# Kernel optimization log

Measured on AMD Instinct MI355X. Metric: run time of the kernel, lower is better.

## Reference

```python
import jax, jax.numpy as jnp
import numpy as np

D_MODEL = 1024
N_HEADS = 16
D_HEAD = 64
TOTAL = N_HEADS * D_HEAD


def setup_inputs() -> dict:
    key = jax.random.key(0)
    k1, k2, k3 = jax.random.split(key, 3)
    x = jax.random.normal(k1, (2, 2048, D_MODEL), dtype=jnp.float32)
    W_qkv = jax.random.normal(k2, (3 * TOTAL, D_MODEL), dtype=jnp.float32) * 0.02
    W_out = jax.random.normal(k3, (D_MODEL, TOTAL), dtype=jnp.float32) * 0.02
    return {"x": x, "W_qkv": W_qkv, "W_out": W_out}


def reference(x, W_qkv, W_out):
    B, T, D = x.shape
    scale = D_HEAD ** -0.5
    qkv = jnp.einsum('btd,ed->bte', x, W_qkv)  # [B,T,3*TOTAL]
    q, k, v = jnp.split(qkv, 3, axis=-1)
    def heads(t):
        return t.reshape(B, T, N_HEADS, D_HEAD).transpose(0, 2, 1, 3)  # [B,H,T,Dh]
    q, k, v = heads(q), heads(k), heads(v)
    scores = jnp.einsum('bhqd,bhkd->bhqk', q, k) * scale
    causal = jnp.tril(jnp.ones((T, T), dtype=bool))
    scores = jnp.where(causal[None, None], scores, -jnp.inf)
    attn = jax.nn.softmax(scores, axis=-1)
    out = jnp.einsum('bhqk,bhkd->bhqd', attn, v)
    out = out.transpose(0, 2, 1, 3).reshape(B, T, TOTAL)
    return jnp.einsum('bte,de->btd', out, W_out)
```

## Files before the change

### kernel.cpp

```cpp
#include <hip/hip_runtime.h>
#include <hip/hip_bf16.h>

typedef __attribute__((ext_vector_type(4))) float f32x4;
typedef __attribute__((ext_vector_type(8))) short s16x8;
typedef __attribute__((ext_vector_type(4))) short s16x4;

#define DEV static __device__ __forceinline__

DEV unsigned short f2bf(float f) {
    unsigned int u = __builtin_bit_cast(unsigned int, f);
    u += 0x7fffu + ((u >> 16) & 1u);
    return (unsigned short)(u >> 16);
}

#if __has_builtin(__builtin_amdgcn_exp2f)
#define EXP2(x) __builtin_amdgcn_exp2f(x)
#else
#define EXP2(x) exp2f(x)
#endif

DEV unsigned int pack2(float a, float b) {
#if __has_builtin(__builtin_amdgcn_perm)
    return __builtin_amdgcn_perm(__builtin_bit_cast(unsigned int, b),
                                 __builtin_bit_cast(unsigned int, a), 0x07060302u);
#else
    return (__builtin_bit_cast(unsigned int, a) >> 16) |
           (__builtin_bit_cast(unsigned int, b) & 0xffff0000u);
#endif
}

DEV s16x8 ld8(const unsigned short* p) {
    s16x4 lo = *(const s16x4*)(p);
    s16x4 hi = *(const s16x4*)(p + 4);
    return __builtin_shufflevector(lo, hi, 0, 1, 2, 3, 4, 5, 6, 7);
}
DEV s16x8 ld8a(const unsigned short* p) { return *(const s16x8*)p; }

DEV f32x4 mfma16(s16x8 a, s16x8 b, f32x4 c) {
    return __builtin_amdgcn_mfma_f32_16x16x32_bf16(a, b, c, 0, 0, 0);
}

DEV void glds16(const unsigned short* g, unsigned short* l) {
    __builtin_amdgcn_global_load_lds(
        (const __attribute__((address_space(1))) unsigned int*)g,
        (__attribute__((address_space(3))) unsigned int*)l, 16, 0, 0);
}

__global__ __launch_bounds__(256) void convf2b2(
        const float* __restrict__ s0, unsigned short* __restrict__ d0, int n40,
        const float* __restrict__ s1, unsigned short* __restrict__ d1, int n41) {
    int i = blockIdx.x * 256 + threadIdx.x;
    if (i < n40) {
        float4 v = ((const float4*)s0)[i];
        s16x4 o = {(short)f2bf(v.x), (short)f2bf(v.y), (short)f2bf(v.z), (short)f2bf(v.w)};
        ((s16x4*)d0)[i] = o;
    } else if (i - n40 < n41) {
        int j = i - n40;
        float4 v = ((const float4*)s1)[j];
        s16x4 o = {(short)f2bf(v.x), (short)f2bf(v.y), (short)f2bf(v.z), (short)f2bf(v.w)};
        ((s16x4*)d1)[j] = o;
    }
}

__global__ __launch_bounds__(256) void convf2b(const float* __restrict__ s,
                                               unsigned short* __restrict__ d, int n4) {
    int i = blockIdx.x * 256 + threadIdx.x;
    if (i < n4) {
        float4 v = ((const float4*)s)[i];
        s16x4 o = {(short)f2bf(v.x), (short)f2bf(v.y), (short)f2bf(v.z), (short)f2bf(v.w)};
        ((s16x4*)d)[i] = o;
    }
}

__global__ __launch_bounds__(256) void qkv_gemm(
        const unsigned short* __restrict__ Xb, const unsigned short* __restrict__ Wq,
        unsigned short* __restrict__ q_ws, unsigned short* __restrict__ k_ws,
        unsigned short* __restrict__ v_ws) {
    __shared__ unsigned short As[2][128 * 32];
    __shared__ unsigned short Bs[2][128 * 32];
    const int tid = threadIdx.x, lane = tid & 63, wave = tid >> 6;
    const int l15 = lane & 15, l4 = lane >> 4;
    const int wm = (wave >> 1) * 64, wn = (wave & 1) * 64;
    const int m0 = blockIdx.y * 128, n0 = blockIdx.x * 128;

    f32x4 acc[4][4];
    for (int i = 0; i < 4; i++)
        for (int j = 0; j < 4; j++) acc[i][j] = (f32x4){0.f, 0.f, 0.f, 0.f};

    const unsigned short* aptr = &Xb[(size_t)(m0 + wave * 32 + (lane >> 2)) * 1024 + (lane & 3) * 8];
    const unsigned short* bptr = &Wq[(size_t)(n0 + wave * 32 + (lane >> 2)) * 1024 + (lane & 3) * 8];

    for (int k0 = 0; k0 < 1024; k0 += 64) {
        __syncthreads();
        for (int c = 0; c < 2; c++) {
            glds16(aptr + k0 + c * 32, &As[c][(wave * 32) * 32]);
            glds16(aptr + k0 + c * 32 + 16 * 1024, &As[c][(wave * 32 + 16) * 32]);
            glds16(bptr + k0 + c * 32, &Bs[c][(wave * 32) * 32]);
            glds16(bptr + k0 + c * 32 + 16 * 1024, &Bs[c][(wave * 32 + 16) * 32]);
        }
        __syncthreads();
        for (int c = 0; c < 2; c++) {
            s16x8 af[4], bf[4];
            for (int mt = 0; mt < 4; mt++) af[mt] = ld8a(&As[c][(wm + mt * 16 + l15) * 32 + l4 * 8]);
            for (int nt = 0; nt < 4; nt++) bf[nt] = ld8a(&Bs[c][(wn + nt * 16 + l15) * 32 + l4 * 8]);
            for (int mt = 0; mt < 4; mt++)
                for (int nt = 0; nt < 4; nt++)
                    acc[mt][nt] = mfma16(af[mt], bf[nt], acc[mt][nt]);
        }
    }

    const int gnb = n0 + wn;
    const int which = gnb >> 10, h = (gnb >> 6) & 15;
    const int bidx = m0 >> 11, tb = m0 & 2047;
    if (which == 2) {
        unsigned short* dst = v_ws + (size_t)(bidx * 16 + h) * 64 * 2048;
        for (int mt = 0; mt < 4; mt++) {
            int t = tb + wm + mt * 16 + l4 * 4;
            for (int nt = 0; nt < 4; nt++) {
                int dh = nt * 16 + l15;
                s16x4 pp;
                for (int r = 0; r < 4; r++) pp[r] = (short)f2bf(acc[mt][nt][r]);
                *(s16x4*)&dst[(size_t)dh * 2048 + t] = pp;
            }
        }
    } else {
        unsigned short* dst = ((which == 0) ? q_ws : k_ws) + (size_t)(bidx * 16 + h) * 2048 * 64;
        const float sc = (which == 0) ? 0.18033688f : 1.0f;
        for (int mt = 0; mt < 4; mt++) {
            int t0 = tb + wm + mt * 16 + l4 * 4;
            for (int nt = 0; nt < 4; nt++) {
                int dh = nt * 16 + l15;
                for (int r = 0; r < 4; r++)
                    dst[(size_t)(t0 + r) * 64 + dh] = f2bf(acc[mt][nt][r] * sc);
            }
        }
    }
}

__global__ __launch_bounds__(256) void attn(
        const unsigned short* __restrict__ q_ws, const unsigned short* __restrict__ k_ws,
        const unsigned short* __restrict__ v_ws, unsigned short* __restrict__ ao) {
    constexpr int LDP = 68;
    __shared__ unsigned short Ks[2][64 * 32];
    __shared__ unsigned short Vt[2][64 * 32];
    __shared__ unsigned short Ps[4 * 32 * LDP];
    const int tid = threadIdx.x, lane = tid & 63, wave = tid >> 6;
    const int l15 = lane & 15, l4 = lane >> 4;
    const int bh = blockIdx.x, b = bh >> 4, h = bh & 15;
    const int q0 = (15 - blockIdx.y) * 128;
    const int qw0 = q0 + wave * 32;
    const size_t base = (size_t)bh * 2048 * 64;
    const unsigned short* vtb = v_ws + (size_t)bh * 64 * 2048;
    unsigned short* Pw = &Ps[wave * 32 * LDP];

    const int hh = wave >> 1, rb = wave & 1;
    const unsigned short* kg0 = &k_ws[base + (size_t)(rb * 32 + (lane >> 2)) * 64 + hh * 32 + (lane & 3) * 8];
    const unsigned short* vg0 = &vtb[(size_t)(rb * 32 + (lane >> 2)) * 2048 + hh * 32 + (lane & 3) * 8];
    unsigned short* kl0 = &Ks[hh][(rb * 32) * 32];
    unsigned short* kl1 = &Ks[hh][(rb * 32 + 16) * 32];
    unsigned short* vl0 = &Vt[hh][(rb * 32) * 32];
    unsigned short* vl1 = &Vt[hh][(rb * 32 + 16) * 32];

    s16x8 qf[2][2];
    for (int qs = 0; qs < 2; qs++)
        for (int c = 0; c < 2; c++)
            qf[qs][c] = ld8a(&q_ws[base + (size_t)(qw0 + qs * 16 + l15) * 64 + c * 32 + l4 * 8]);

    f32x4 o[4][2];
    for (int i = 0; i < 4; i++)
        for (int j = 0; j < 2; j++) o[i][j] = (f32x4){0.f, 0.f, 0.f, 0.f};
    float lsum[2] = {0.f, 0.f};

    const int kend = q0 + 128;
    for (int k0 = 0; k0 < kend; k0 += 64) {
        __syncthreads();
        glds16(kg0 + (size_t)k0 * 64, kl0);
        glds16(kg0 + (size_t)(k0 + 16) * 64, kl1);
        glds16(vg0 + k0, vl0);
        glds16(vg0 + k0 + 16 * 2048, vl1);
        __syncthreads();

        if (k0 < qw0 + 32) {
            f32x4 st[4][2];
            for (int ks = 0; ks < 4; ks++)
                for (int qs = 0; qs < 2; qs++) st[ks][qs] = (f32x4){0.f, 0.f, 0.f, 0.f};
            for (int c = 0; c < 2; c++)
                for (int ks = 0; ks < 4; ks++) {
                    s16x8 kf = ld8a(&Ks[c][(ks * 16 + l15) * 32 + l4 * 8]);
                    st[ks][0] = mfma16(kf, qf[0][c], st[ks][0]);
                    st[ks][1] = mfma16(kf, qf[1][c], st[ks][1]);
                }

            for (int qs = 0; qs < 2; qs++) {
                if (k0 + 63 > qw0 + qs * 16) {
                    int qg = qw0 + qs * 16 + l15;
                    for (int ks = 0; ks < 4; ks++)
                        for (int r = 0; r < 4; r++) {
                            int kg = k0 + ks * 16 + l4 * 4 + r;
                            if (kg > qg) st[ks][qs][r] = -1e30f;
                        }
                }
                float part = 0.f;
                for (int ks = 0; ks < 4; ks++) {
                    float p0 = EXP2(st[ks][qs][0]);
                    float p1 = EXP2(st[ks][qs][1]);
                    float p2 = EXP2(st[ks][qs][2]);
                    float p3 = EXP2(st[ks][qs][3]);
                    part += (p0 + p1) + (p2 + p3);
                    unsigned int u0 = pack2(p0, p1), u1 = pack2(p2, p3);
                    *(uint2*)&Pw[(qs * 16 + l15) * LDP + ks * 16 + l4 * 4] = (uint2){u0, u1};
                }
                lsum[qs] += part;
            }

            s16x8 pf[2][2];
            for (int qs = 0; qs < 2; qs++)
                for (int c = 0; c < 2; c++)
                    pf[qs][c] = ld8(&Pw[(qs * 16 + l15) * LDP + c * 32 + l4 * 8]);
            for (int c = 0; c < 2; c++)
                for (int ds = 0; ds < 4; ds++) {
                    s16x8 vf = ld8a(&Vt[c][(ds * 16 + l15) * 32 + l4 * 8]);
                    o[ds][0] = mfma16(vf, pf[0][c], o[ds][0]);
                    o[ds][1] = mfma16(vf, pf[1][c], o[ds][1]);
                }
        }
    }

    float inv[2];
    for (int qs = 0; qs < 2; qs++) {
        float t = lsum[qs];
        t += __shfl_xor(t, 16, 64);
        t += __shfl_xor(t, 32, 64);
        inv[qs] = 1.f / t;
    }
    for (int ds = 0; ds < 4; ds++)
        for (int qs = 0; qs < 2; qs++) {
            s16x4 pp;
            for (int r = 0; r < 4; r++) pp[r] = (short)f2bf(o[ds][qs][r] * inv[qs]);
            *(s16x4*)&Pw[(qs * 16 + l15) * LDP + ds * 16 + l4 * 4] = pp;
        }
    int qr = lane >> 1, half = lane & 1;
    size_t orow = ((size_t)b * 2048 + q0 + wave * 32 + qr) * 1024 + h * 64 + half * 32;
    for (int j = 0; j < 4; j++) {
        s16x8 vv = ld8(&Pw[qr * LDP + half * 32 + j * 8]);
        *(s16x8*)&ao[orow + j * 8] = vv;
    }
}

__global__ __launch_bounds__(256) void out_gemm(
        const unsigned short* __restrict__ A, const unsigned short* __restrict__ Bm,
        float* __restrict__ OUT) {
    __shared__ unsigned short As[2][128 * 32];
    __shared__ unsigned short Bs[2][128 * 32];
    const int tid = threadIdx.x, lane = tid & 63, wave = tid >> 6;
    const int l15 = lane & 15, l4 = lane >> 4;
    const int wm = (wave >> 1) * 64, wn = (wave & 1) * 64;
    const int m0 = blockIdx.y * 128, n0 = blockIdx.x * 128;

    f32x4 acc[4][4];
    for (int i = 0; i < 4; i++)
        for (int j = 0; j < 4; j++) acc[i][j] = (f32x4){0.f, 0.f, 0.f, 0.f};

    const unsigned short* aptr = &A[(size_t)(m0 + wave * 32 + (lane >> 2)) * 1024 + (lane & 3) * 8];
    const unsigned short* bptr = &Bm[(size_t)(n0 + wave * 32 + (lane >> 2)) * 1024 + (lane & 3) * 8];

    for (int k0 = 0; k0 < 1024; k0 += 64) {
        __syncthreads();
        for (int c = 0; c < 2; c++) {
            glds16(aptr + k0 + c * 32, &As[c][(wave * 32) * 32]);
            glds16(aptr + k0 + c * 32 + 16 * 1024, &As[c][(wave * 32 + 16) * 32]);
            glds16(bptr + k0 + c * 32, &Bs[c][(wave * 32) * 32]);
            glds16(bptr + k0 + c * 32 + 16 * 1024, &Bs[c][(wave * 32 + 16) * 32]);
        }
        __syncthreads();
        for (int c = 0; c < 2; c++) {
            s16x8 af[4], bf[4];
            for (int mt = 0; mt < 4; mt++) af[mt] = ld8a(&As[c][(wm + mt * 16 + l15) * 32 + l4 * 8]);
            for (int nt = 0; nt < 4; nt++) bf[nt] = ld8a(&Bs[c][(wn + nt * 16 + l15) * 32 + l4 * 8]);
            for (int mt = 0; mt < 4; mt++)
                for (int nt = 0; nt < 4; nt++)
                    acc[mt][nt] = mfma16(af[mt], bf[nt], acc[mt][nt]);
        }
    }

    for (int mt = 0; mt < 4; mt++)
        for (int nt = 0; nt < 4; nt++)
            for (int r = 0; r < 4; r++) {
                int gm = m0 + wm + mt * 16 + l4 * 4 + r;
                int gn = n0 + wn + nt * 16 + l15;
                OUT[(size_t)gm * 1024 + gn] = acc[mt][nt][r];
            }
}

extern "C" void kernel_launch(void* const* d_in, const int* in_sizes, int n_in,
                              void* d_out, int out_size, void* d_ws, size_t ws_size,
                              hipStream_t stream) {
    (void)in_sizes; (void)n_in; (void)out_size; (void)ws_size;
    const float* x    = (const float*)d_in[0];
    const float* Wqkv = (const float*)d_in[1];
    const float* Wout = (const float*)d_in[2];
    float* out = (float*)d_out;

    unsigned short* q_ws = (unsigned short*)d_ws;
    unsigned short* k_ws = q_ws + (size_t)4 * 1024 * 1024;
    unsigned short* v_ws = k_ws + (size_t)4 * 1024 * 1024;
    unsigned short* xb   = v_ws + (size_t)4 * 1024 * 1024;
    unsigned short* ao   = xb;
    unsigned short* wqb  = (unsigned short*)d_out;
    unsigned short* wob  = q_ws;

    const int n4x = 2 * 2048 * 1024 / 4, n4w = 3072 * 1024 / 4;
    convf2b2<<<(n4x + n4w + 255) / 256, 256, 0, stream>>>(x, xb, n4x, Wqkv, wqb, n4w);
    qkv_gemm<<<dim3(24, 32), 256, 0, stream>>>(xb, wqb, q_ws, k_ws, v_ws);
    attn<<<dim3(32, 16), 256, 0, stream>>>(q_ws, k_ws, v_ws, ao);
    convf2b<<<1024, 256, 0, stream>>>(Wout, wob, 1024 * 1024 / 4);
    out_gemm<<<dim3(8, 32), 256, 0, stream>>>(ao, wob, out);
}
```

Measured before the change: 195.2 us.

## Split attention block across eight waves with 16 query rows each

The attention kernel now runs 512 threads per block, with each of eight waves owning 16 query rows instead of four waves owning 32. The K/V tile load is spread across twice as many waves, so each lane issues half the global-to-LDS copies, and per-wave registers shrink. This is meant to raise parallelism and latency hiding and to cut causal waste, since waves skip tiles at a finer granularity. In exchange, every wave rereads the K/V fragments from LDS for only half the MFMA work, so LDS read traffic per FLOP doubles.

New measurement: 190.6 us. 1.02x faster.

```diff
diff --git a/kernel.cpp b/kernel.cpp
--- a/kernel.cpp
+++ b/kernel.cpp
@@ -137,114 +137,96 @@
     }
 }
 
-__global__ __launch_bounds__(256) void attn(
+__global__ __launch_bounds__(512) void attn(
         const unsigned short* __restrict__ q_ws, const unsigned short* __restrict__ k_ws,
         const unsigned short* __restrict__ v_ws, unsigned short* __restrict__ ao) {
     constexpr int LDP = 68;
     __shared__ unsigned short Ks[2][64 * 32];
     __shared__ unsigned short Vt[2][64 * 32];
-    __shared__ unsigned short Ps[4 * 32 * LDP];
+    __shared__ unsigned short Ps[8 * 16 * LDP];
     const int tid = threadIdx.x, lane = tid & 63, wave = tid >> 6;
     const int l15 = lane & 15, l4 = lane >> 4;
     const int bh = blockIdx.x, b = bh >> 4, h = bh & 15;
     const int q0 = (15 - blockIdx.y) * 128;
-    const int qw0 = q0 + wave * 32;
+    const int qw0 = q0 + wave * 16;
     const size_t base = (size_t)bh * 2048 * 64;
     const unsigned short* vtb = v_ws + (size_t)bh * 64 * 2048;
-    unsigned short* Pw = &Ps[wave * 32 * LDP];
-
-    const int hh = wave >> 1, rb = wave & 1;
-    const unsigned short* kg0 = &k_ws[base + (size_t)(rb * 32 + (lane >> 2)) * 64 + hh * 32 + (lane & 3) * 8];
-    const unsigned short* vg0 = &vtb[(size_t)(rb * 32 + (lane >> 2)) * 2048 + hh * 32 + (lane & 3) * 8];
-    unsigned short* kl0 = &Ks[hh][(rb * 32) * 32];
-    unsigned short* kl1 = &Ks[hh][(rb * 32 + 16) * 32];
-    unsigned short* vl0 = &Vt[hh][(rb * 32) * 32];
-    unsigned short* vl1 = &Vt[hh][(rb * 32 + 16) * 32];
-
-    s16x8 qf[2][2];
-    for (int qs = 0; qs < 2; qs++)
-        for (int c = 0; c < 2; c++)
-            qf[qs][c] = ld8a(&q_ws[base + (size_t)(qw0 + qs * 16 + l15) * 64 + c * 32 + l4 * 8]);
-
-    f32x4 o[4][2];
-    for (int i = 0; i < 4; i++)
-        for (int j = 0; j < 2; j++) o[i][j] = (f32x4){0.f, 0.f, 0.f, 0.f};
-    float lsum[2] = {0.f, 0.f};
+    unsigned short* Pw = &Ps[wave * 16 * LDP];
+
+    const int seg = wave & 3, half = wave >> 2;
+    const unsigned short* kg0 = &k_ws[base + (size_t)(seg * 16 + (lane >> 2)) * 64 + half * 32 + (lane & 3) * 8];
+    const unsigned short* vg0 = &vtb[(size_t)(seg * 16 + (lane >> 2)) * 2048 + half * 32 + (lane & 3) * 8];
+    unsigned short* kl = &Ks[half][(seg * 16) * 32];
+    unsigned short* vl = &Vt[half][(seg * 16) * 32];
+
+    s16x8 qf[2];
+    for (int c = 0; c < 2; c++)
+        qf[c] = ld8a(&q_ws[base + (size_t)(qw0 + l15) * 64 + c * 32 + l4 * 8]);
+
+    f32x4 o[4];
+    for (int i = 0; i < 4; i++) o[i] = (f32x4){0.f, 0.f, 0.f, 0.f};
+    float lsum = 0.f;
 
     const int kend = q0 + 128;
     for (int k0 = 0; k0 < kend; k0 += 64) {
         __syncthreads();
-        glds16(kg0 + (size_t)k0 * 64, kl0);
-        glds16(kg0 + (size_t)(k0 + 16) * 64, kl1);
-        glds16(vg0 + k0, vl0);
-        glds16(vg0 + k0 + 16 * 2048, vl1);
-        __syncthreads();
-
-        if (k0 < qw0 + 32) {
-            f32x4 st[4][2];
-            for (int ks = 0; ks < 4; ks++)
-                for (int qs = 0; qs < 2; qs++) st[ks][qs] = (f32x4){0.f, 0.f, 0.f, 0.f};
+        glds16(kg0 + (size_t)k0 * 64, kl);
+        glds16(vg0 + k0, vl);
+        __syncthreads();
+
+        if (k0 < qw0 + 16) {
+            f32x4 st[4];
+            for (int ks = 0; ks < 4; ks++) st[ks] = (f32x4){0.f, 0.f, 0.f, 0.f};
             for (int c = 0; c < 2; c++)
                 for (int ks = 0; ks < 4; ks++) {
                     s16x8 kf = ld8a(&Ks[c][(ks * 16 + l15) * 32 + l4 * 8]);
-                    st[ks][0] = mfma16(kf, qf[0][c], st[ks][0]);
-                    st[ks][1] = mfma16(kf, qf[1][c], st[ks][1]);
+                    st[ks] = mfma16(kf, qf[c], st[ks]);
                 }
 
-            for (int qs = 0; qs < 2; qs++) {
-                if (k0 + 63 > qw0 + qs * 16) {
-                    int qg = qw0 + qs * 16 + l15;
-                    for (int ks = 0; ks < 4; ks++)
-                        for (int r = 0; r < 4; r++) {
-                            int kg = k0 + ks * 16 + l4 * 4 + r;
-                            if (kg > qg) st[ks][qs][r] = -1e30f;
-                        }
-                }
-                float part = 0.f;
-                for (int ks = 0; ks < 4; ks++) {
-                    float p0 = EXP2(st[ks][qs][0]);
-                    float p1 = EXP2(st[ks][qs][1]);
-                    float p2 = EXP2(st[ks][qs][2]);
-                    float p3 = EXP2(st[ks][qs][3]);
-                    part += (p0 + p1) + (p2 + p3);
-                    unsigned int u0 = pack2(p0, p1), u1 = pack2(p2, p3);
-                    *(uint2*)&Pw[(qs * 16 + l15) * LDP + ks * 16 + l4 * 4] = (uint2){u0, u1};
-                }
-                lsum[qs] += part;
-            }
-
-            s16x8 pf[2][2];
-            for (int qs = 0; qs < 2; qs++)
-                for (int c = 0; c < 2; c++)
-                    pf[qs][c] = ld8(&Pw[(qs * 16 + l15) * LDP + c * 32 + l4 * 8]);
+            if (k0 + 63 > qw0) {
+                int qg = qw0 + l15;
+                for (int ks = 0; ks < 4; ks++)
+                    for (int r = 0; r < 4; r++) {
+                        int kg = k0 + ks * 16 + l4 * 4 + r;
+                        if (kg > qg) st[ks][r] = -1e30f;
+                    }
+            }
+            float part = 0.f;
+            for (int ks = 0; ks < 4; ks++) {
+                float p0 = EXP2(st[ks][0]);
+                float p1 = EXP2(st[ks][1]);
+                float p2 = EXP2(st[ks][2]);
+                float p3 = EXP2(st[ks][3]);
+                part += (p0 + p1) + (p2 + p3);
+                unsigned int u0 = pack2(p0, p1), u1 = pack2(p2, p3);
+                *(uint2*)&Pw[l15 * LDP + ks * 16 + l4 * 4] = (uint2){u0, u1};
+            }
+            lsum += part;
+
+            s16x8 pf[2];
+            for (int c = 0; c < 2; c++)
+                pf[c] = ld8(&Pw[l15 * LDP + c * 32 + l4 * 8]);
             for (int c = 0; c < 2; c++)
                 for (int ds = 0; ds < 4; ds++) {
                     s16x8 vf = ld8a(&Vt[c][(ds * 16 + l15) * 32 + l4 * 8]);
-                    o[ds][0] = mfma16(vf, pf[0][c], o[ds][0]);
-                    o[ds][1] = mfma16(vf, pf[1][c], o[ds][1]);
+                    o[ds] = mfma16(vf, pf[c], o[ds]);
                 }
         }
     }
 
-    float inv[2];
-    for (int qs = 0; qs < 2; qs++) {
-        float t = lsum[qs];
-        t += __shfl_xor(t, 16, 64);
-        t += __shfl_xor(t, 32, 64);
-        inv[qs] = 1.f / t;
-    }
-    for (int ds = 0; ds < 4; ds++)
-        for (int qs = 0; qs < 2; qs++) {
-            s16x4 pp;
-            for (int r = 0; r < 4; r++) pp[r] = (short)f2bf(o[ds][qs][r] * inv[qs]);
-            *(s16x4*)&Pw[(qs * 16 + l15) * LDP + ds * 16 + l4 * 4] = pp;
-        }
-    int qr = lane >> 1, half = lane & 1;
-    size_t orow = ((size_t)b * 2048 + q0 + wave * 32 + qr) * 1024 + h * 64 + half * 32;
-    for (int j = 0; j < 4; j++) {
-        s16x8 vv = ld8(&Pw[qr * LDP + half * 32 + j * 8]);
-        *(s16x8*)&ao[orow + j * 8] = vv;
-    }
+    float t = lsum;
+    t += __shfl_xor(t, 16, 64);
+    t += __shfl_xor(t, 32, 64);
+    float inv = 1.f / t;
+    for (int ds = 0; ds < 4; ds++) {
+        s16x4 pp;
+        for (int r = 0; r < 4; r++) pp[r] = (short)f2bf(o[ds][r] * inv);
+        *(s16x4*)&Pw[l15 * LDP + ds * 16 + l4 * 4] = pp;
+    }
+    int qr = lane >> 2, qt = lane & 3;
+    size_t orow = ((size_t)b * 2048 + q0 + wave * 16 + qr) * 1024 + h * 64 + qt * 16;
+    *(s16x8*)&ao[orow]     = ld8(&Pw[qr * LDP + qt * 16]);
+    *(s16x8*)&ao[orow + 8] = ld8(&Pw[qr * LDP + qt * 16 + 8]);
 }
 
 __global__ __launch_bounds__(256) void out_gemm(
@@ -312,7 +294,7 @@
     const int n4x = 2 * 2048 * 1024 / 4, n4w = 3072 * 1024 / 4;
     convf2b2<<<(n4x + n4w + 255) / 256, 256, 0, stream>>>(x, xb, n4x, Wqkv, wqb, n4w);
     qkv_gemm<<<dim3(24, 32), 256, 0, stream>>>(xb, wqb, q_ws, k_ws, v_ws);
-    attn<<<dim3(32, 16), 256, 0, stream>>>(q_ws, k_ws, v_ws, ao);
+    attn<<<dim3(32, 16), 512, 0, stream>>>(q_ws, k_ws, v_ws, ao);
     convf2b<<<1024, 256, 0, stream>>>(Wout, wob, 1024 * 1024 / 4);
     out_gemm<<<dim3(8, 32), 256, 0, stream>>>(ao, wob, out);
 }
```
